# Kernel tuning notes

Measured on AMD Instinct MI355X. Metric: run time of the kernel, lower is better.

## Reference

```python
import jax, jax.numpy as jnp
import numpy as np

IN_F, HID, OUT_F = 171, 1024, 171

def _cond_lst(condition_num, groundtruth_num, seq_len):
    num_cycles = seq_len // (condition_num + groundtruth_num) + 1
    lst = np.zeros((num_cycles, condition_num + groundtruth_num), dtype=np.float32)
    lst[:, :groundtruth_num] = 1.0
    return lst.reshape(-1)[:seq_len]

def setup_inputs() -> dict:
    key = jax.random.key(0)
    ks = jax.random.split(key, 16)
    s = 0.02
    inp = {
        'real_seq': jax.random.normal(ks[0], (128, 128, IN_F), jnp.float32),
        'W_ih1': jax.random.normal(ks[1], (4 * HID, IN_F), jnp.float32) * s,
        'W_hh1': jax.random.normal(ks[2], (4 * HID, HID), jnp.float32) * s,
        'b_ih1': jnp.zeros((4 * HID,), jnp.float32),
        'b_hh1': jnp.zeros((4 * HID,), jnp.float32),
        'W_ih2': jax.random.normal(ks[3], (4 * HID, HID), jnp.float32) * s,
        'W_hh2': jax.random.normal(ks[4], (4 * HID, HID), jnp.float32) * s,
        'b_ih2': jnp.zeros((4 * HID,), jnp.float32),
        'b_hh2': jnp.zeros((4 * HID,), jnp.float32),
        'W_ih3': jax.random.normal(ks[5], (4 * HID, HID), jnp.float32) * s,
        'W_hh3': jax.random.normal(ks[6], (4 * HID, HID), jnp.float32) * s,
        'b_ih3': jnp.zeros((4 * HID,), jnp.float32),
        'b_hh3': jnp.zeros((4 * HID,), jnp.float32),
        'W_dec': jax.random.normal(ks[7], (OUT_F, HID), jnp.float32) * s,
        'b_dec': jnp.zeros((OUT_F,), jnp.float32),
        'condition_num': 5,
        'groundtruth_num': 5,
    }
    return inp

def _lstm_cell(x, h, c, Wih, Whh, bih, bhh):
    # PyTorch LSTMCell: gates ordered i, f, g, o
    g = x @ Wih.T + bih + h @ Whh.T + bhh
    i, f, gg, o = jnp.split(g, 4, axis=-1)
    c2 = jax.nn.sigmoid(f) * c + jax.nn.sigmoid(i) * jnp.tanh(gg)
    h2 = jax.nn.sigmoid(o) * jnp.tanh(c2)
    return h2, c2

def reference(real_seq, W_ih1, W_hh1, b_ih1, b_hh1, W_ih2, W_hh2, b_ih2, b_hh2,
              W_ih3, W_hh3, b_ih3, b_hh3, W_dec, b_dec, condition_num, groundtruth_num):
    B, T, _ = real_seq.shape
    cond = jnp.asarray(_cond_lst(condition_num, groundtruth_num, T))  # [T], 1=use ground truth
    z = jnp.zeros((B, HID), jnp.float32)
    carry0 = (z, z, z, z, z, z, jnp.zeros((B, OUT_F), jnp.float32))
    xs = (jnp.swapaxes(real_seq, 0, 1), cond)  # time-major

    def step(carry, x):
        h0, h1, h2, c0, c1, c2, out_frame = carry
        frame, c_flag = x
        in_frame = jnp.where(c_flag > 0.5, frame, out_frame)
        h0, c0 = _lstm_cell(in_frame, h0, c0, W_ih1, W_hh1, b_ih1, b_hh1)
        h1, c1 = _lstm_cell(h0, h1, c1, W_ih2, W_hh2, b_ih2, b_hh2)
        h2, c2 = _lstm_cell(h1, h2, c2, W_ih3, W_hh3, b_ih3, b_hh3)
        out_frame = h2 @ W_dec.T + b_dec
        return (h0, h1, h2, c0, c1, c2, out_frame), out_frame

    _, out_seq = jax.lax.scan(step, carry0, xs)  # [T, B, OUT_F]
    return jnp.swapaxes(out_seq, 0, 1)  # [B, T, OUT_F]
```

## Files before the change

### kernel.cpp

```cpp
#include <hip/hip_runtime.h>

#define TT 128
#define INF 171

typedef _Float16 half8 __attribute__((ext_vector_type(8)));
typedef float floatx4 __attribute__((ext_vector_type(4)));
typedef unsigned short u16;

#define XBSZ 163840
#define HSZ  131072

#define WAITV(n) asm volatile("s_waitcnt vmcnt(" #n ")" ::: "memory")
#define SCHEDB() __builtin_amdgcn_sched_barrier(0)

__device__ __forceinline__ u16 f2h(float f){
  _Float16 h = (_Float16)f;
  return __builtin_bit_cast(u16, h);
}
__device__ __forceinline__ float sigm(float x){ return 1.f/(1.f+__expf(-x)); }
__device__ __forceinline__ float tanh_(float x){ return 1.f - 2.f/(__expf(2.f*x)+1.f); }

__device__ __forceinline__ void scat_coh(u16* buf, int nch, int b, int k, u16 v){
  u16* p = buf + (size_t)((((b>>4)*nch + (k>>5))*4 + ((k>>3)&3))*16 + (b&15))*8 + (k&7);
  unsigned int vv = v;
  asm volatile("global_store_short %0, %1, off sc0 sc1" :: "v"(p), "v"(vv) : "memory");
}
__device__ __forceinline__ void ld16_coh(half8& d, const u16* p){
  asm volatile("global_load_dwordx4 %0, %1, off sc0 sc1" : "=&v"(d) : "v"(p) : "memory");
}

template<int NB>
__device__ __forceinline__ void issue_pair(const u16* s0, const u16* s1,
    half8* v, int tid, int beat0){
  #pragma unroll
  for (int i=0;i<NB;i++) ld16_coh(v[i],    s0 + (size_t)(beat0+i)*4096 + (size_t)tid*8);
  #pragma unroll
  for (int i=0;i<NB;i++) ld16_coh(v[NB+i], s1 + (size_t)(beat0+i)*4096 + (size_t)tid*8);
}

__global__ __launch_bounds__(256) void prep_w1f(const float* __restrict__ Wih1,
    const float* __restrict__ Whh1, u16* __restrict__ Wf){
  int u = blockIdx.x*256 + threadIdx.x;
  int tile = u / 2560;
  int r = u - tile*2560;
  int kc = r >> 6, l = r & 63;
  int row = (tile>>6)*1024 + (tile&63)*16 + (l&15);
  int k0 = kc*32 + ((l>>4)<<3);
  half8 hv;
  #pragma unroll
  for (int e=0;e<8;e++){
    int k = k0+e;
    float w = 0.f;
    if (k < 171)       w = Wih1[(size_t)row*171 + k];
    else if (k < 1195) w = Whh1[(size_t)row*1024 + (k-171)];
    hv[e] = (_Float16)w;
  }
  *(half8*)&Wf[(size_t)(tile*40 + kc)*512 + (size_t)l*8] = hv;
}

__global__ __launch_bounds__(256) void prep_w23f(const float* __restrict__ Wih2,
    const float* __restrict__ Whh2, const float* __restrict__ Wih3,
    const float* __restrict__ Whh3, u16* __restrict__ W2f, u16* __restrict__ W3f){
  int u = blockIdx.x*256 + threadIdx.x;
  int tile = u >> 12;
  int r = u & 4095;
  int kc = r >> 6, l = r & 63;
  int row = (tile>>6)*1024 + (tile&63)*16 + (l&15);
  int k0 = kc*32 + ((l>>4)<<3);
  half8 h2, h3;
  #pragma unroll
  for (int e=0;e<8;e++){
    int k = k0+e;
    size_t si = (size_t)row*1024 + (k & 1023);
    h2[e] = (_Float16)((k < 1024) ? Wih2[si] : Whh2[si]);
    h3[e] = (_Float16)((k < 1024) ? Wih3[si] : Whh3[si]);
  }
  size_t base = (size_t)(tile*64 + kc)*512 + (size_t)l*8;
  *(half8*)&W2f[base] = h2;
  *(half8*)&W3f[base] = h3;
}

__global__ __launch_bounds__(256) void prep_wdecf(const float* __restrict__ Wdec,
    u16* __restrict__ Wdf){
  int u = blockIdx.x*256 + threadIdx.x;
  int tile = u / 2048;
  int r = u & 2047;
  int kc = r >> 6, l = r & 63;
  int row = tile*16 + (l&15);
  int k0 = kc*32 + ((l>>4)<<3);
  half8 hv;
  #pragma unroll
  for (int e=0;e<8;e++){
    int k = k0+e;
    hv[e] = (_Float16)((row < 171) ? Wdec[(size_t)row*1024 + k] : 0.f);
  }
  *(half8*)&Wdf[(size_t)(tile*32 + kc)*512 + (size_t)l*8] = hv;
}

__global__ __launch_bounds__(256) void prep_misc(
    const float* __restrict__ rseq, const int* __restrict__ gnp,
    const float* __restrict__ bih1, const float* __restrict__ bhh1,
    const float* __restrict__ bih2, const float* __restrict__ bhh2,
    const float* __restrict__ bih3, const float* __restrict__ bhh3,
    const float* __restrict__ bdec,
    u16* __restrict__ Xb1f, u16* __restrict__ Hf, float* __restrict__ cbuf,
    float* __restrict__ b1, float* __restrict__ b2, float* __restrict__ b3,
    float* __restrict__ bd, int* __restrict__ bar)
{
  size_t idx = (size_t)blockIdx.x*256 + threadIdx.x;
  if (idx < 327680){
    int q = (int)(idx / 163840);
    int rem = (int)(idx % 163840);
    int btile = rem / 20480;
    int r2 = rem % 20480;
    int kc = r2 >> 9, r3 = r2 & 511;
    int l = r3 >> 3, e = r3 & 7;
    int b = btile*16 + (l&15);
    int k = kc*32 + ((l>>4)<<3) + e;
    float v = 0.f;
    if (q==0 && k < 171 && *gnp > 0) v = rseq[(size_t)b*TT*INF + k];
    Xb1f[idx] = f2h(v);
    return;
  }
  idx -= 327680;
  if (idx < 786432){ Hf[idx] = 0; return; }
  idx -= 786432;
  if (idx < 393216){ cbuf[idx] = 0.f; return; }
  idx -= 393216;
  if (idx < 12288){
    int which = (int)(idx >> 12), j = (int)(idx & 4095);
    float v = (which==0)? (bih1[j]+bhh1[j]) : (which==1)? (bih2[j]+bhh2[j]) : (bih3[j]+bhh3[j]);
    ((which==0)?b1:(which==1)?b2:b3)[j] = v;
    return;
  }
  idx -= 12288;
  if (idx < 176){ bd[idx] = (idx < 171) ? bdec[idx] : 0.f; return; }
  idx -= 176;
  if (idx < 512) bar[idx] = 0;
}

__device__ __forceinline__ void gridbar(int* __restrict__ bar, int cls, int hv,
                                        int bc, int* s_dead){
  __syncthreads();
  if (threadIdx.x == 0 && !(*s_dead)){
    int* arr = &bar[cls*64 + hv*32];
    int* gen = &bar[256 + cls*32];
    bool released = false;
    int o = __hip_atomic_fetch_add(arr, 1, __ATOMIC_RELAXED, __HIP_MEMORY_SCOPE_AGENT);
    if ((o & 31) == 31){
      int og = __hip_atomic_fetch_add(gen, 1, __ATOMIC_RELAXED, __HIP_MEMORY_SCOPE_AGENT);
      released = (og & 1) == 1;
    }
    if (!released){
      long long t0 = clock64();
      while (__hip_atomic_load(gen, __ATOMIC_RELAXED, __HIP_MEMORY_SCOPE_AGENT) < 2*(bc+1)){
        __builtin_amdgcn_s_sleep(2);
        if (clock64() - t0 > 30000000LL){ *s_dead = 1; break; }
      }
    }
  }
  __syncthreads();
}

template<int KHALF, int GS, bool NT>
__device__ __forceinline__ void gemm_stream(const u16* __restrict__ wp,
    const u16* __restrict__ x0, const u16* __restrict__ x1,
    floatx4& a0, floatx4& a1)
{
  constexpr int NG = KHALF/GS;
  half8 W[2][GS];
  #pragma unroll
  for (int i=0;i<GS;i++)
    W[0][i] = NT ? __builtin_nontemporal_load((const half8*)(wp + (size_t)i*512))
                 : *(const half8*)(wp + (size_t)i*512);
  #pragma unroll
  for (int g8=0; g8<NG; g8++){
    const int cur = g8 & 1, nxt = cur ^ 1;
    if (g8+1 < NG){
      const size_t off = (size_t)(g8+1)*GS*512;
      #pragma unroll
      for (int i=0;i<GS;i++)
        W[nxt][i] = NT ? __builtin_nontemporal_load((const half8*)(wp + off + (size_t)i*512))
                       : *(const half8*)(wp + off + (size_t)i*512);
    }
    #pragma unroll
    for (int i=0;i<GS;i++){
      half8 xv0 = *(const half8*)(x0 + (size_t)(g8*GS+i)*512);
      half8 xv1 = *(const half8*)(x1 + (size_t)(g8*GS+i)*512);
      a0 = __builtin_amdgcn_mfma_f32_16x16x32_f16(W[cur][i], xv0, a0, 0,0,0);
      a1 = __builtin_amdgcn_mfma_f32_16x16x32_f16(W[cur][i], xv1, a1, 0,0,0);
    }
  }
}

__global__ void __launch_bounds__(512,2) acro_persist(
    const u16* __restrict__ W1f, const u16* __restrict__ W2f,
    const u16* __restrict__ W3f, const u16* __restrict__ Wdf,
    u16* __restrict__ Xb1f, u16* __restrict__ Hf,
    const float* __restrict__ b1, const float* __restrict__ b2,
    const float* __restrict__ b3, const float* __restrict__ bd,
    const float* __restrict__ rseq, float* __restrict__ out,
    const int* __restrict__ cnp, const int* __restrict__ gnp, int* __restrict__ bar)
{
  __shared__ u16 XL[65536];
  __shared__ float gb[8][16][33];
  __shared__ int s_dead;
  const int bId = (int)blockIdx.x;
  const int js = (bId & 7)*8 + ((bId >> 5) & 7);
  const int nq = (bId >> 3) & 3;
  const int bh = (bId >> 5) & 1;
  const int tid = (int)threadIdx.x;
  const int w = tid >> 6, l = tid & 63;
  const int g = w >> 1, hf = w & 1;
  const int l15 = l & 15, lq = l >> 4;
  const int uu = tid >> 5, bq = tid & 31;
  const int jj = js*16 + uu, bgg = nq*32 + bq;
  if (tid == 0) s_dead = 0;
  const int gnv = *gnp;
  int P = *cnp + gnv; if (P < 1) P = 1;
  int bc = 0;

  u16* H0[2] = { Hf,          Hf + HSZ   };
  u16* H1[2] = { Hf + 2*HSZ,  Hf + 3*HSZ };
  u16* H2[2] = { Hf + 4*HSZ,  Hf + 5*HSZ };

  float bs1[4], bs2[4], bs3[4];
  #pragma unroll
  for (int q=0;q<4;q++){
    bs1[q] = b1[q*1024 + jj];
    bs2[q] = b2[q*1024 + jj];
    bs3[q] = b3[q*1024 + jj];
  }
  const bool dec_act = (js < 11);
  const int oo = js*16 + uu;
  const float bdr = dec_act ? bd[oo] : 0.f;
  float c0r = 0.f, c1r = 0.f, c2r = 0.f;

  half8 pf1[8], pf2[8], pf3[8];
  issue_pair<4>(Xb1f + (size_t)(nq*2  )*20480,
                Xb1f + (size_t)(nq*2+1)*20480, pf1, tid, 1);

  __syncthreads();
  for (int t=0; t<TT; t++){
    const int pr = t & 1, nx = pr ^ 1;

    {
      const u16* xb = Xb1f + (size_t)pr*XBSZ;
      half8 fr0, fr1;
      ld16_coh(fr0, xb + (size_t)(nq*2  )*20480 + (size_t)tid*8);
      ld16_coh(fr1, xb + (size_t)(nq*2+1)*20480 + (size_t)tid*8);
      WAITV(0);
      SCHEDB();
      *(half8*)&XL[(size_t)tid*8] = fr0;
      *(half8*)&XL[(size_t)5*4096 + (size_t)tid*8] = fr1;
      #pragma unroll
      for (int i=0;i<4;i++){
        *(half8*)&XL[(size_t)(1+i)*4096 + (size_t)tid*8] = pf1[i];
        *(half8*)&XL[(size_t)(6+i)*4096 + (size_t)tid*8] = pf1[4+i];
      }
      __syncthreads();
      const u16* wp = W1f + ((size_t)(g*64 + js)*40 + (size_t)hf*20)*512 + (size_t)(l<<3);
      const u16* x0 = XL + (size_t)hf*10240 + (size_t)(l<<3);
      const u16* x1 = x0 + 20480;
      floatx4 a0{}, a1{};
      gemm_stream<20,4,false>(wp, x0, x1, a0, a1);
      #pragma unroll
      for (int r=0;r<4;r++){
        gb[w][lq*4+r][l15]      = a0[r];
        gb[w][lq*4+r][16 + l15] = a1[r];
      }
      __syncthreads();
      {
        float gi = gb[0][uu][bq] + gb[1][uu][bq] + bs1[0];
        float gf = gb[2][uu][bq] + gb[3][uu][bq] + bs1[1];
        float gg = gb[4][uu][bq] + gb[5][uu][bq] + bs1[2];
        float go = gb[6][uu][bq] + gb[7][uu][bq] + bs1[3];
        float c = sigm(gf)*c0r + sigm(gi)*tanh_(gg);
        c0r = c;
        u16 hb = f2h(sigm(go)*tanh_(c));
        scat_coh(H0[pr], 32, bgg, jj, hb);
        scat_coh(Xb1f + (size_t)nx*XBSZ, 40, bgg, 171 + jj, hb);
      }
      issue_pair<4>(H1[nx] + (size_t)(nq*2  )*16384,
                    H1[nx] + (size_t)(nq*2+1)*16384, pf2, tid, 0);
    }
    WAITV(8);
    gridbar(bar, nq, bh, bc, &s_dead); bc++;

    {
      half8 fr[8];
      issue_pair<4>(H0[pr] + (size_t)(nq*2  )*16384,
                    H0[pr] + (size_t)(nq*2+1)*16384, fr, tid, 0);
      WAITV(0);
      SCHEDB();
      #pragma unroll
      for (int i=0;i<8;i++) *(half8*)&XL[(size_t)i*4096 + (size_t)tid*8] = fr[i];
      #pragma unroll
      for (int i=0;i<8;i++) *(half8*)&XL[32768 + (size_t)i*4096 + (size_t)tid*8] = pf2[i];
      __syncthreads();
      const u16* wp = W2f + ((size_t)(g*64 + js)*64 + (size_t)hf*32)*512 + (size_t)(l<<3);
      const u16* x0 = XL + (size_t)hf*32768 + (size_t)(l<<3);
      const u16* x1 = x0 + 16384;
      floatx4 a0{}, a1{};
      gemm_stream<32,8,false>(wp, x0, x1, a0, a1);
      #pragma unroll
      for (int r=0;r<4;r++){
        gb[w][lq*4+r][l15]      = a0[r];
        gb[w][lq*4+r][16 + l15] = a1[r];
      }
      __syncthreads();
      {
        float gi = gb[0][uu][bq] + gb[1][uu][bq] + bs2[0];
        float gf = gb[2][uu][bq] + gb[3][uu][bq] + bs2[1];
        float gg = gb[4][uu][bq] + gb[5][uu][bq] + bs2[2];
        float go = gb[6][uu][bq] + gb[7][uu][bq] + bs2[3];
        float c = sigm(gf)*c1r + sigm(gi)*tanh_(gg);
        c1r = c;
        u16 hb = f2h(sigm(go)*tanh_(c));
        scat_coh(H1[pr], 32, bgg, jj, hb);
      }
      issue_pair<4>(H2[nx] + (size_t)(nq*2  )*16384,
                    H2[nx] + (size_t)(nq*2+1)*16384, pf3, tid, 0);
    }
    WAITV(8);
    gridbar(bar, nq, bh, bc, &s_dead); bc++;

    {
      half8 fr[8];
      issue_pair<4>(H1[pr] + (size_t)(nq*2  )*16384,
                    H1[pr] + (size_t)(nq*2+1)*16384, fr, tid, 0);
      WAITV(0);
      SCHEDB();
      #pragma unroll
      for (int i=0;i<8;i++) *(half8*)&XL[(size_t)i*4096 + (size_t)tid*8] = fr[i];
      #pragma unroll
      for (int i=0;i<8;i++) *(half8*)&XL[32768 + (size_t)i*4096 + (size_t)tid*8] = pf3[i];
      __syncthreads();
      const u16* wp = W3f + ((size_t)(g*64 + js)*64 + (size_t)hf*32)*512 + (size_t)(l<<3);
      const u16* x0 = XL + (size_t)hf*32768 + (size_t)(l<<3);
      const u16* x1 = x0 + 16384;
      floatx4 a0{}, a1{};
      gemm_stream<32,8,true>(wp, x0, x1, a0, a1);
      #pragma unroll
      for (int r=0;r<4;r++){
        gb[w][lq*4+r][l15]      = a0[r];
        gb[w][lq*4+r][16 + l15] = a1[r];
      }
      __syncthreads();
      {
        float gi = gb[0][uu][bq] + gb[1][uu][bq] + bs3[0];
        float gf = gb[2][uu][bq] + gb[3][uu][bq] + bs3[1];
        float gg = gb[4][uu][bq] + gb[5][uu][bq] + bs3[2];
        float go = gb[6][uu][bq] + gb[7][uu][bq] + bs3[3];
        float c = sigm(gf)*c2r + sigm(gi)*tanh_(gg);
        c2r = c;
        u16 hb = f2h(sigm(go)*tanh_(c));
        scat_coh(H2[pr], 32, bgg, jj, hb);
      }
    }
    WAITV(0);
    gridbar(bar, nq, bh, bc, &s_dead); bc++;

    if (dec_act){
      half8 fd[8];
      issue_pair<4>(H2[pr] + (size_t)(nq*2  )*16384,
                    H2[pr] + (size_t)(nq*2+1)*16384, fd, tid, 0);
      WAITV(0);
      SCHEDB();
      #pragma unroll
      for (int i=0;i<8;i++) *(half8*)&XL[(size_t)i*4096 + (size_t)tid*8] = fd[i];
      __syncthreads();
      const u16* wp = Wdf + (size_t)(js*32 + w*4)*512 + (size_t)(l<<3);
      const u16* x0 = XL + (size_t)(w*4)*512 + (size_t)(l<<3);
      const u16* x1 = x0 + 16384;
      floatx4 d0{}, d1{};
      #pragma unroll
      for (int i=0;i<4;i++){
        half8 wv  = *(const half8*)(wp + (size_t)i*512);
        half8 a0v = *(const half8*)(x0 + (size_t)i*512);
        half8 a1v = *(const half8*)(x1 + (size_t)i*512);
        d0 = __builtin_amdgcn_mfma_f32_16x16x32_f16(wv, a0v, d0, 0,0,0);
        d1 = __builtin_amdgcn_mfma_f32_16x16x32_f16(wv, a1v, d1, 0,0,0);
      }
      #pragma unroll
      for (int r=0;r<4;r++){
        gb[w][lq*4+r][l15]      = d0[r];
        gb[w][lq*4+r][16 + l15] = d1[r];
      }
      __syncthreads();
      const int nf = (((t+1) % P) < gnv) ? 1 : 0;
      if (oo < 171){
        float v = bdr;
        #pragma unroll
        for (int i=0;i<8;i++) v += gb[i][uu][bq];
        out[((size_t)bgg*TT + t)*INF + oo] = v;
        if (t+1 < TT){
          float src = nf ? rseq[((size_t)bgg*TT + (t+1))*INF + oo] : v;
          scat_coh(Xb1f + (size_t)nx*XBSZ, 40, bgg, oo, f2h(src));
        }
      }
    }
    if (t+1 < TT){
      const u16* xbn = Xb1f + (size_t)nx*XBSZ;
      issue_pair<4>(xbn + (size_t)(nq*2  )*20480,
                    xbn + (size_t)(nq*2+1)*20480, pf1, tid, 1);
      WAITV(8);
    } else {
      WAITV(0);
    }
    gridbar(bar, nq, bh, bc, &s_dead); bc++;
  }
}

extern "C" void kernel_launch(void* const* d_in, const int* in_sizes, int n_in,
                              void* d_out, int out_size, void* d_ws, size_t ws_size,
                              hipStream_t stream)
{
  const float* rseq = (const float*)d_in[0];
  const float* Wih1 = (const float*)d_in[1];
  const float* Whh1 = (const float*)d_in[2];
  const float* bih1 = (const float*)d_in[3];
  const float* bhh1 = (const float*)d_in[4];
  const float* Wih2 = (const float*)d_in[5];
  const float* Whh2 = (const float*)d_in[6];
  const float* bih2 = (const float*)d_in[7];
  const float* bhh2 = (const float*)d_in[8];
  const float* Wih3 = (const float*)d_in[9];
  const float* Whh3 = (const float*)d_in[10];
  const float* bih3 = (const float*)d_in[11];
  const float* bhh3 = (const float*)d_in[12];
  const float* Wdec = (const float*)d_in[13];
  const float* bdec = (const float*)d_in[14];
  const int* cn = (const int*)d_in[15];
  const int* gn = (const int*)d_in[16];
  float* out = (float*)d_out;

  char* p = (char*)d_ws;
  auto take = [&](size_t n){ void* r = (void*)p; p += (n + 255) & ~(size_t)255; return r; };
  u16* W1f  = (u16*)take(5242880UL*2);
  u16* W2f  = (u16*)take(8388608UL*2);
  u16* W3f  = (u16*)take(8388608UL*2);
  u16* Wdf  = (u16*)take(180224UL*2);
  u16* Xb1f = (u16*)take(327680UL*2);
  u16* Hf   = (u16*)take(786432UL*2);
  float* cbuf = (float*)take(393216UL*4);
  float* b1 = (float*)take(4096*4);
  float* b2 = (float*)take(4096*4);
  float* b3 = (float*)take(4096*4);
  float* bd = (float*)take(176*4);
  int* bar  = (int*)take(512*4);
  if ((size_t)(p - (char*)d_ws) > ws_size) return;

  prep_w1f  <<<2560,256,0,stream>>>(Wih1, Whh1, W1f);
  prep_w23f <<<4096,256,0,stream>>>(Wih2, Whh2, Wih3, Whh3, W2f, W3f);
  prep_wdecf<<<88,  256,0,stream>>>(Wdec, Wdf);
  prep_misc <<<5939,256,0,stream>>>(rseq, gn, bih1,bhh1,bih2,bhh2,bih3,bhh3,bdec,
                                    Xb1f, Hf, cbuf, b1,b2,b3,bd, bar);

  acro_persist<<<256,512,0,stream>>>(W1f, W2f, W3f, Wdf, Xb1f, Hf,
                                     b1, b2, b3, bd, rseq, out, cn, gn, bar);
}
```

Baseline: 4.867 ms.

## Split persistent LSTM grid into 512 blocks each owning 16 batch rows

```diff
diff --git a/kernel.cpp b/kernel.cpp
--- a/kernel.cpp
+++ b/kernel.cpp
@@ -10,7 +10,7 @@
 #define XBSZ 163840
 #define HSZ  131072
 
-#define WAITV(n) asm volatile("s_waitcnt vmcnt(" #n ")" ::: "memory")
+#define WAITV0() asm volatile("s_waitcnt vmcnt(0)" ::: "memory")
 #define SCHEDB() __builtin_amdgcn_sched_barrier(0)
 
 __device__ __forceinline__ u16 f2h(float f){
@@ -27,15 +27,6 @@
 }
 __device__ __forceinline__ void ld16_coh(half8& d, const u16* p){
   asm volatile("global_load_dwordx4 %0, %1, off sc0 sc1" : "=&v"(d) : "v"(p) : "memory");
-}
-
-template<int NB>
-__device__ __forceinline__ void issue_pair(const u16* s0, const u16* s1,
-    half8* v, int tid, int beat0){
-  #pragma unroll
-  for (int i=0;i<NB;i++) ld16_coh(v[i],    s0 + (size_t)(beat0+i)*4096 + (size_t)tid*8);
-  #pragma unroll
-  for (int i=0;i<NB;i++) ld16_coh(v[NB+i], s1 + (size_t)(beat0+i)*4096 + (size_t)tid*8);
 }
 
 __global__ __launch_bounds__(256) void prep_w1f(const float* __restrict__ Wih1,
@@ -136,15 +127,15 @@
   idx -= 12288;
   if (idx < 176){ bd[idx] = (idx < 171) ? bdec[idx] : 0.f; return; }
   idx -= 176;
-  if (idx < 512) bar[idx] = 0;
+  if (idx < 1024) bar[idx] = 0;
 }
 
 __device__ __forceinline__ void gridbar(int* __restrict__ bar, int cls, int hv,
                                         int bc, int* s_dead){
   __syncthreads();
   if (threadIdx.x == 0 && !(*s_dead)){
-    int* arr = &bar[cls*64 + hv*32];
-    int* gen = &bar[256 + cls*32];
+    int* arr = &bar[(cls*2 + hv)*32];
+    int* gen = &bar[512 + cls*32];
     bool released = false;
     int o = __hip_atomic_fetch_add(arr, 1, __ATOMIC_RELAXED, __HIP_MEMORY_SCOPE_AGENT);
     if ((o & 31) == 31){
@@ -162,17 +153,39 @@
   __syncthreads();
 }
 
-template<int KHALF, int GS, bool NT>
-__device__ __forceinline__ void gemm_stream(const u16* __restrict__ wp,
-    const u16* __restrict__ x0, const u16* __restrict__ x1,
-    floatx4& a0, floatx4& a1)
+template<int NB>
+__device__ __forceinline__ void stage_n(const u16* s0, u16* XL, int tid, int lb0){
+  half8 v[NB];
+  #pragma unroll
+  for (int i=0;i<NB;i++) ld16_coh(v[i], s0 + (size_t)i*4096 + (size_t)tid*8);
+  WAITV0();
+  SCHEDB();
+  #pragma unroll
+  for (int i=0;i<NB;i++) *(half8*)&XL[(size_t)(lb0+i)*4096 + (size_t)tid*8] = v[i];
+}
+__device__ __forceinline__ void stage_44(const u16* sf, const u16* ss,
+                                         u16* XL, int tid){
+  half8 v[8];
+  #pragma unroll
+  for (int i=0;i<4;i++) ld16_coh(v[i],   sf + (size_t)i*4096 + (size_t)tid*8);
+  #pragma unroll
+  for (int i=0;i<4;i++) ld16_coh(v[4+i], ss + (size_t)i*4096 + (size_t)tid*8);
+  WAITV0();
+  SCHEDB();
+  #pragma unroll
+  for (int i=0;i<8;i++) *(half8*)&XL[(size_t)i*4096 + (size_t)tid*8] = v[i];
+}
+
+template<int KHALF>
+__device__ __forceinline__ void gemm1(const u16* __restrict__ wp,
+    const u16* __restrict__ x0, floatx4& a0)
 {
+  constexpr int GS = 4;
   constexpr int NG = KHALF/GS;
   half8 W[2][GS];
   #pragma unroll
   for (int i=0;i<GS;i++)
-    W[0][i] = NT ? __builtin_nontemporal_load((const half8*)(wp + (size_t)i*512))
-                 : *(const half8*)(wp + (size_t)i*512);
+    W[0][i] = *(const half8*)(wp + (size_t)i*512);
   #pragma unroll
   for (int g8=0; g8<NG; g8++){
     const int cur = g8 & 1, nxt = cur ^ 1;
@@ -180,20 +193,17 @@
       const size_t off = (size_t)(g8+1)*GS*512;
       #pragma unroll
       for (int i=0;i<GS;i++)
-        W[nxt][i] = NT ? __builtin_nontemporal_load((const half8*)(wp + off + (size_t)i*512))
-                       : *(const half8*)(wp + off + (size_t)i*512);
+        W[nxt][i] = *(const half8*)(wp + off + (size_t)i*512);
     }
     #pragma unroll
     for (int i=0;i<GS;i++){
       half8 xv0 = *(const half8*)(x0 + (size_t)(g8*GS+i)*512);
-      half8 xv1 = *(const half8*)(x1 + (size_t)(g8*GS+i)*512);
       a0 = __builtin_amdgcn_mfma_f32_16x16x32_f16(W[cur][i], xv0, a0, 0,0,0);
-      a1 = __builtin_amdgcn_mfma_f32_16x16x32_f16(W[cur][i], xv1, a1, 0,0,0);
-    }
-  }
-}
-
-__global__ void __launch_bounds__(512,2) acro_persist(
+    }
+  }
+}
+
+__global__ void __launch_bounds__(512,4) acro_persist(
     const u16* __restrict__ W1f, const u16* __restrict__ W2f,
     const u16* __restrict__ W3f, const u16* __restrict__ Wdf,
     u16* __restrict__ Xb1f, u16* __restrict__ Hf,
@@ -202,19 +212,23 @@
     const float* __restrict__ rseq, float* __restrict__ out,
     const int* __restrict__ cnp, const int* __restrict__ gnp, int* __restrict__ bar)
 {
-  __shared__ u16 XL[65536];
-  __shared__ float gb[8][16][33];
+  __shared__ u16 XL[32768];
+  __shared__ float gb[8][16][17];
   __shared__ int s_dead;
   const int bId = (int)blockIdx.x;
-  const int js = (bId & 7)*8 + ((bId >> 5) & 7);
-  const int nq = (bId >> 3) & 3;
-  const int bh = (bId >> 5) & 1;
+  const int lo = bId & 255;
+  const int js = (lo & 7)*8 + ((lo >> 5) & 7);
+  const int q2 = (lo >> 3) & 3;
+  const int half = bId >> 8;
+  const int ct = q2*2 + half;
+  const int hv = (lo >> 5) & 1;
   const int tid = (int)threadIdx.x;
   const int w = tid >> 6, l = tid & 63;
   const int g = w >> 1, hf = w & 1;
   const int l15 = l & 15, lq = l >> 4;
-  const int uu = tid >> 5, bq = tid & 31;
-  const int jj = js*16 + uu, bgg = nq*32 + bq;
+  const int uu = (tid >> 4) & 15, bq = tid & 15;
+  const bool ep = (tid < 256);
+  const int jj = js*16 + uu, bgg = ct*16 + bq;
   if (tid == 0) s_dead = 0;
   const int gnv = *gnp;
   int P = *cnp + gnv; if (P < 1) P = 1;
@@ -232,45 +246,32 @@
     bs3[q] = b3[q*1024 + jj];
   }
   const bool dec_act = (js < 11);
-  const int oo = js*16 + uu;
+  const int oo = jj;
   const float bdr = dec_act ? bd[oo] : 0.f;
   float c0r = 0.f, c1r = 0.f, c2r = 0.f;
 
-  half8 pf1[8], pf2[8], pf3[8];
-  issue_pair<4>(Xb1f + (size_t)(nq*2  )*20480,
-                Xb1f + (size_t)(nq*2+1)*20480, pf1, tid, 1);
+  const size_t xoff = (size_t)ct*20480;
+  const size_t hoff = (size_t)ct*16384;
+
+  const u16* wp1 = W1f + ((size_t)(g*64 + js)*40 + (size_t)hf*20)*512 + (size_t)(l<<3);
+  const u16* wp2 = W2f + ((size_t)(g*64 + js)*64 + (size_t)hf*32)*512 + (size_t)(l<<3);
+  const u16* wp3 = W3f + ((size_t)(g*64 + js)*64 + (size_t)hf*32)*512 + (size_t)(l<<3);
+  const u16* wpd = Wdf + (size_t)(js*32 + w*4)*512 + (size_t)(l<<3);
 
   __syncthreads();
   for (int t=0; t<TT; t++){
     const int pr = t & 1, nx = pr ^ 1;
 
     {
-      const u16* xb = Xb1f + (size_t)pr*XBSZ;
-      half8 fr0, fr1;
-      ld16_coh(fr0, xb + (size_t)(nq*2  )*20480 + (size_t)tid*8);
-      ld16_coh(fr1, xb + (size_t)(nq*2+1)*20480 + (size_t)tid*8);
-      WAITV(0);
-      SCHEDB();
-      *(half8*)&XL[(size_t)tid*8] = fr0;
-      *(half8*)&XL[(size_t)5*4096 + (size_t)tid*8] = fr1;
-      #pragma unroll
-      for (int i=0;i<4;i++){
-        *(half8*)&XL[(size_t)(1+i)*4096 + (size_t)tid*8] = pf1[i];
-        *(half8*)&XL[(size_t)(6+i)*4096 + (size_t)tid*8] = pf1[4+i];
-      }
-      __syncthreads();
-      const u16* wp = W1f + ((size_t)(g*64 + js)*40 + (size_t)hf*20)*512 + (size_t)(l<<3);
+      stage_n<5>(Xb1f + (size_t)pr*XBSZ + xoff, XL, tid, 0);
+      __syncthreads();
       const u16* x0 = XL + (size_t)hf*10240 + (size_t)(l<<3);
-      const u16* x1 = x0 + 20480;
-      floatx4 a0{}, a1{};
-      gemm_stream<20,4,false>(wp, x0, x1, a0, a1);
-      #pragma unroll
-      for (int r=0;r<4;r++){
-        gb[w][lq*4+r][l15]      = a0[r];
-        gb[w][lq*4+r][16 + l15] = a1[r];
-      }
-      __syncthreads();
-      {
+      floatx4 a0{};
+      gemm1<20>(wp1, x0, a0);
+      #pragma unroll
+      for (int r=0;r<4;r++) gb[w][lq*4+r][l15] = a0[r];
+      __syncthreads();
+      if (ep){
         float gi = gb[0][uu][bq] + gb[1][uu][bq] + bs1[0];
         float gf = gb[2][uu][bq] + gb[3][uu][bq] + bs1[1];
         float gg = gb[4][uu][bq] + gb[5][uu][bq] + bs1[2];
@@ -281,35 +282,20 @@
         scat_coh(H0[pr], 32, bgg, jj, hb);
         scat_coh(Xb1f + (size_t)nx*XBSZ, 40, bgg, 171 + jj, hb);
       }
-      issue_pair<4>(H1[nx] + (size_t)(nq*2  )*16384,
-                    H1[nx] + (size_t)(nq*2+1)*16384, pf2, tid, 0);
-    }
-    WAITV(8);
-    gridbar(bar, nq, bh, bc, &s_dead); bc++;
+    }
+    WAITV0();
+    gridbar(bar, ct, hv, bc, &s_dead); bc++;
 
     {
-      half8 fr[8];
-      issue_pair<4>(H0[pr] + (size_t)(nq*2  )*16384,
-                    H0[pr] + (size_t)(nq*2+1)*16384, fr, tid, 0);
-      WAITV(0);
-      SCHEDB();
-      #pragma unroll
-      for (int i=0;i<8;i++) *(half8*)&XL[(size_t)i*4096 + (size_t)tid*8] = fr[i];
-      #pragma unroll
-      for (int i=0;i<8;i++) *(half8*)&XL[32768 + (size_t)i*4096 + (size_t)tid*8] = pf2[i];
-      __syncthreads();
-      const u16* wp = W2f + ((size_t)(g*64 + js)*64 + (size_t)hf*32)*512 + (size_t)(l<<3);
-      const u16* x0 = XL + (size_t)hf*32768 + (size_t)(l<<3);
-      const u16* x1 = x0 + 16384;
-      floatx4 a0{}, a1{};
-      gemm_stream<32,8,false>(wp, x0, x1, a0, a1);
-      #pragma unroll
-      for (int r=0;r<4;r++){
-        gb[w][lq*4+r][l15]      = a0[r];
-        gb[w][lq*4+r][16 + l15] = a1[r];
-      }
-      __syncthreads();
-      {
+      stage_44(H0[pr] + hoff, H1[nx] + hoff, XL, tid);
+      __syncthreads();
+      const u16* x0 = XL + (size_t)hf*16384 + (size_t)(l<<3);
+      floatx4 a0{};
+      gemm1<32>(wp2, x0, a0);
+      #pragma unroll
+      for (int r=0;r<4;r++) gb[w][lq*4+r][l15] = a0[r];
+      __syncthreads();
+      if (ep){
         float gi = gb[0][uu][bq] + gb[1][uu][bq] + bs2[0];
         float gf = gb[2][uu][bq] + gb[3][uu][bq] + bs2[1];
         float gg = gb[4][uu][bq] + gb[5][uu][bq] + bs2[2];
@@ -319,35 +305,20 @@
         u16 hb = f2h(sigm(go)*tanh_(c));
         scat_coh(H1[pr], 32, bgg, jj, hb);
       }
-      issue_pair<4>(H2[nx] + (size_t)(nq*2  )*16384,
-                    H2[nx] + (size_t)(nq*2+1)*16384, pf3, tid, 0);
-    }
-    WAITV(8);
-    gridbar(bar, nq, bh, bc, &s_dead); bc++;
+    }
+    WAITV0();
+    gridbar(bar, ct, hv, bc, &s_dead); bc++;
 
     {
-      half8 fr[8];
-      issue_pair<4>(H1[pr] + (size_t)(nq*2  )*16384,
-                    H1[pr] + (size_t)(nq*2+1)*16384, fr, tid, 0);
-      WAITV(0);
-      SCHEDB();
-      #pragma unroll
-      for (int i=0;i<8;i++) *(half8*)&XL[(size_t)i*4096 + (size_t)tid*8] = fr[i];
-      #pragma unroll
-      for (int i=0;i<8;i++) *(half8*)&XL[32768 + (size_t)i*4096 + (size_t)tid*8] = pf3[i];
-      __syncthreads();
-      const u16* wp = W3f + ((size_t)(g*64 + js)*64 + (size_t)hf*32)*512 + (size_t)(l<<3);
-      const u16* x0 = XL + (size_t)hf*32768 + (size_t)(l<<3);
-      const u16* x1 = x0 + 16384;
-      floatx4 a0{}, a1{};
-      gemm_stream<32,8,true>(wp, x0, x1, a0, a1);
-      #pragma unroll
-      for (int r=0;r<4;r++){
-        gb[w][lq*4+r][l15]      = a0[r];
-        gb[w][lq*4+r][16 + l15] = a1[r];
-      }
-      __syncthreads();
-      {
+      stage_44(H1[pr] + hoff, H2[nx] + hoff, XL, tid);
+      __syncthreads();
+      const u16* x0 = XL + (size_t)hf*16384 + (size_t)(l<<3);
+      floatx4 a0{};
+      gemm1<32>(wp3, x0, a0);
+      #pragma unroll
+      for (int r=0;r<4;r++) gb[w][lq*4+r][l15] = a0[r];
+      __syncthreads();
+      if (ep){
         float gi = gb[0][uu][bq] + gb[1][uu][bq] + bs3[0];
         float gf = gb[2][uu][bq] + gb[3][uu][bq] + bs3[1];
         float gg = gb[4][uu][bq] + gb[5][uu][bq] + bs3[2];
@@ -358,38 +329,25 @@
         scat_coh(H2[pr], 32, bgg, jj, hb);
       }
     }
-    WAITV(0);
-    gridbar(bar, nq, bh, bc, &s_dead); bc++;
+    WAITV0();
+    gridbar(bar, ct, hv, bc, &s_dead); bc++;
 
     if (dec_act){
-      half8 fd[8];
-      issue_pair<4>(H2[pr] + (size_t)(nq*2  )*16384,
-                    H2[pr] + (size_t)(nq*2+1)*16384, fd, tid, 0);
-      WAITV(0);
-      SCHEDB();
-      #pragma unroll
-      for (int i=0;i<8;i++) *(half8*)&XL[(size_t)i*4096 + (size_t)tid*8] = fd[i];
-      __syncthreads();
-      const u16* wp = Wdf + (size_t)(js*32 + w*4)*512 + (size_t)(l<<3);
+      stage_n<4>(H2[pr] + hoff, XL, tid, 0);
+      __syncthreads();
       const u16* x0 = XL + (size_t)(w*4)*512 + (size_t)(l<<3);
-      const u16* x1 = x0 + 16384;
-      floatx4 d0{}, d1{};
+      floatx4 d0{};
       #pragma unroll
       for (int i=0;i<4;i++){
-        half8 wv  = *(const half8*)(wp + (size_t)i*512);
+        half8 wv  = *(const half8*)(wpd + (size_t)i*512);
         half8 a0v = *(const half8*)(x0 + (size_t)i*512);
-        half8 a1v = *(const half8*)(x1 + (size_t)i*512);
         d0 = __builtin_amdgcn_mfma_f32_16x16x32_f16(wv, a0v, d0, 0,0,0);
-        d1 = __builtin_amdgcn_mfma_f32_16x16x32_f16(wv, a1v, d1, 0,0,0);
-      }
-      #pragma unroll
-      for (int r=0;r<4;r++){
-        gb[w][lq*4+r][l15]      = d0[r];
-        gb[w][lq*4+r][16 + l15] = d1[r];
-      }
+      }
+      #pragma unroll
+      for (int r=0;r<4;r++) gb[w][lq*4+r][l15] = d0[r];
       __syncthreads();
       const int nf = (((t+1) % P) < gnv) ? 1 : 0;
-      if (oo < 171){
+      if (ep && oo < 171){
         float v = bdr;
         #pragma unroll
         for (int i=0;i<8;i++) v += gb[i][uu][bq];
@@ -400,15 +358,8 @@
         }
       }
     }
-    if (t+1 < TT){
-      const u16* xbn = Xb1f + (size_t)nx*XBSZ;
-      issue_pair<4>(xbn + (size_t)(nq*2  )*20480,
-                    xbn + (size_t)(nq*2+1)*20480, pf1, tid, 1);
-      WAITV(8);
-    } else {
-      WAITV(0);
-    }
-    gridbar(bar, nq, bh, bc, &s_dead); bc++;
+    WAITV0();
+    gridbar(bar, ct, hv, bc, &s_dead); bc++;
   }
 }
 
@@ -448,15 +399,15 @@
   float* b2 = (float*)take(4096*4);
   float* b3 = (float*)take(4096*4);
   float* bd = (float*)take(176*4);
-  int* bar  = (int*)take(512*4);
+  int* bar  = (int*)take(1024*4);
   if ((size_t)(p - (char*)d_ws) > ws_size) return;
 
   prep_w1f  <<<2560,256,0,stream>>>(Wih1, Whh1, W1f);
   prep_w23f <<<4096,256,0,stream>>>(Wih2, Whh2, Wih3, Whh3, W2f, W3f);
   prep_wdecf<<<88,  256,0,stream>>>(Wdec, Wdf);
-  prep_misc <<<5939,256,0,stream>>>(rseq, gn, bih1,bhh1,bih2,bhh2,bih3,bhh3,bdec,
+  prep_misc <<<5941,256,0,stream>>>(rseq, gn, bih1,bhh1,bih2,bhh2,bih3,bhh3,bdec,
                                     Xb1f, Hf, cbuf, b1,b2,b3,bd, bar);
 
-  acro_persist<<<256,512,0,stream>>>(W1f, W2f, W3f, Wdf, Xb1f, Hf,
+  acro_persist<<<512,512,0,stream>>>(W1f, W2f, W3f, Wdf, Xb1f, Hf,
                                      b1, b2, b3, bd, rseq, out, cn, gn, bar);
 }
```

Result: slower. 6.210 ms (+27.6%).

## Prefetch next layer's weights across grid barriers using a 4-deep register ring

Applied to the files above, without the earlier changes.

```diff
diff --git a/kernel.cpp b/kernel.cpp
--- a/kernel.cpp
+++ b/kernel.cpp
@@ -28,6 +28,9 @@
 __device__ __forceinline__ void ld16_coh(half8& d, const u16* p){
   asm volatile("global_load_dwordx4 %0, %1, off sc0 sc1" : "=&v"(d) : "v"(p) : "memory");
 }
+__device__ __forceinline__ void ld16_c(half8& d, const u16* p){
+  asm volatile("global_load_dwordx4 %0, %1, off" : "=&v"(d) : "v"(p) : "memory");
+}
 
 template<int NB>
 __device__ __forceinline__ void issue_pair(const u16* s0, const u16* s1,
@@ -36,6 +39,15 @@
   for (int i=0;i<NB;i++) ld16_coh(v[i],    s0 + (size_t)(beat0+i)*4096 + (size_t)tid*8);
   #pragma unroll
   for (int i=0;i<NB;i++) ld16_coh(v[NB+i], s1 + (size_t)(beat0+i)*4096 + (size_t)tid*8);
+}
+
+template<bool COH>
+__device__ __forceinline__ void wgrp(half8* Ws, const u16* wp, int grp){
+  #pragma unroll
+  for (int i=0;i<4;i++){
+    const u16* p = wp + (size_t)grp*2048 + (size_t)i*512;
+    if (COH) ld16_coh(Ws[i], p); else ld16_c(Ws[i], p);
+  }
 }
 
 __global__ __launch_bounds__(256) void prep_w1f(const float* __restrict__ Wih1,
@@ -162,34 +174,29 @@
   __syncthreads();
 }
 
-template<int KHALF, int GS, bool NT>
-__device__ __forceinline__ void gemm_stream(const u16* __restrict__ wp,
+template<int NG, bool COH>
+__device__ __forceinline__ void gemm_ring(const u16* __restrict__ wp,
     const u16* __restrict__ x0, const u16* __restrict__ x1,
-    floatx4& a0, floatx4& a1)
+    floatx4& a0, floatx4& a1, half8 (&W)[4][4])
 {
-  constexpr int NG = KHALF/GS;
-  half8 W[2][GS];
-  #pragma unroll
-  for (int i=0;i<GS;i++)
-    W[0][i] = NT ? __builtin_nontemporal_load((const half8*)(wp + (size_t)i*512))
-                 : *(const half8*)(wp + (size_t)i*512);
-  #pragma unroll
-  for (int g8=0; g8<NG; g8++){
-    const int cur = g8 & 1, nxt = cur ^ 1;
-    if (g8+1 < NG){
-      const size_t off = (size_t)(g8+1)*GS*512;
-      #pragma unroll
-      for (int i=0;i<GS;i++)
-        W[nxt][i] = NT ? __builtin_nontemporal_load((const half8*)(wp + off + (size_t)i*512))
-                       : *(const half8*)(wp + off + (size_t)i*512);
+  #pragma unroll
+  for (int g=0; g<NG; g++){
+    if (g >= 2){
+      const int rem = (g+4 <= NG-1) ? 3 : (NG-1-g);
+      if (rem >= 3)      { WAITV(12); }
+      else if (rem == 2) { WAITV(8); }
+      else if (rem == 1) { WAITV(4); }
+      else               { WAITV(0); }
+      SCHEDB();
     }
     #pragma unroll
-    for (int i=0;i<GS;i++){
-      half8 xv0 = *(const half8*)(x0 + (size_t)(g8*GS+i)*512);
-      half8 xv1 = *(const half8*)(x1 + (size_t)(g8*GS+i)*512);
-      a0 = __builtin_amdgcn_mfma_f32_16x16x32_f16(W[cur][i], xv0, a0, 0,0,0);
-      a1 = __builtin_amdgcn_mfma_f32_16x16x32_f16(W[cur][i], xv1, a1, 0,0,0);
-    }
+    for (int i=0;i<4;i++){
+      half8 xv0 = *(const half8*)(x0 + (size_t)(g*4+i)*512);
+      half8 xv1 = *(const half8*)(x1 + (size_t)(g*4+i)*512);
+      a0 = __builtin_amdgcn_mfma_f32_16x16x32_f16(W[g&3][i], xv0, a0, 0,0,0);
+      a1 = __builtin_amdgcn_mfma_f32_16x16x32_f16(W[g&3][i], xv1, a1, 0,0,0);
+    }
+    if (g+4 < NG) wgrp<COH>(W[g&3], wp, g+4);
   }
 }
 
@@ -224,6 +231,11 @@
   u16* H1[2] = { Hf + 2*HSZ,  Hf + 3*HSZ };
   u16* H2[2] = { Hf + 4*HSZ,  Hf + 5*HSZ };
 
+  const u16* wp1 = W1f + ((size_t)(g*64 + js)*40 + (size_t)hf*20)*512 + (size_t)(l<<3);
+  const u16* wp2 = W2f + ((size_t)(g*64 + js)*64 + (size_t)hf*32)*512 + (size_t)(l<<3);
+  const u16* wp3 = W3f + ((size_t)(g*64 + js)*64 + (size_t)hf*32)*512 + (size_t)(l<<3);
+  const u16* wpd = Wdf + (size_t)(js*32 + w*4)*512 + (size_t)(l<<3);
+
   float bs1[4], bs2[4], bs3[4];
   #pragma unroll
   for (int q=0;q<4;q++){
@@ -237,8 +249,11 @@
   float c0r = 0.f, c1r = 0.f, c2r = 0.f;
 
   half8 pf1[8], pf2[8], pf3[8];
+  half8 Wr[4][4];
   issue_pair<4>(Xb1f + (size_t)(nq*2  )*20480,
                 Xb1f + (size_t)(nq*2+1)*20480, pf1, tid, 1);
+  wgrp<false>(Wr[0], wp1, 0);
+  wgrp<false>(Wr[1], wp1, 1);
 
   __syncthreads();
   for (int t=0; t<TT; t++){
@@ -249,7 +264,9 @@
       half8 fr0, fr1;
       ld16_coh(fr0, xb + (size_t)(nq*2  )*20480 + (size_t)tid*8);
       ld16_coh(fr1, xb + (size_t)(nq*2+1)*20480 + (size_t)tid*8);
-      WAITV(0);
+      wgrp<false>(Wr[2], wp1, 2);
+      wgrp<false>(Wr[3], wp1, 3);
+      WAITV(8);
       SCHEDB();
       *(half8*)&XL[(size_t)tid*8] = fr0;
       *(half8*)&XL[(size_t)5*4096 + (size_t)tid*8] = fr1;
@@ -259,11 +276,10 @@
         *(half8*)&XL[(size_t)(6+i)*4096 + (size_t)tid*8] = pf1[4+i];
       }
       __syncthreads();
-      const u16* wp = W1f + ((size_t)(g*64 + js)*40 + (size_t)hf*20)*512 + (size_t)(l<<3);
       const u16* x0 = XL + (size_t)hf*10240 + (size_t)(l<<3);
       const u16* x1 = x0 + 20480;
       floatx4 a0{}, a1{};
-      gemm_stream<20,4,false>(wp, x0, x1, a0, a1);
+      gemm_ring<5,false>(wp1, x0, x1, a0, a1, Wr);
       #pragma unroll
       for (int r=0;r<4;r++){
         gb[w][lq*4+r][l15]      = a0[r];
@@ -283,26 +299,29 @@
       }
       issue_pair<4>(H1[nx] + (size_t)(nq*2  )*16384,
                     H1[nx] + (size_t)(nq*2+1)*16384, pf2, tid, 0);
-    }
-    WAITV(8);
+      wgrp<false>(Wr[0], wp2, 0);
+      wgrp<false>(Wr[1], wp2, 1);
+    }
+    WAITV(16);
     gridbar(bar, nq, bh, bc, &s_dead); bc++;
 
     {
       half8 fr[8];
       issue_pair<4>(H0[pr] + (size_t)(nq*2  )*16384,
                     H0[pr] + (size_t)(nq*2+1)*16384, fr, tid, 0);
-      WAITV(0);
+      wgrp<false>(Wr[2], wp2, 2);
+      wgrp<false>(Wr[3], wp2, 3);
+      WAITV(8);
       SCHEDB();
       #pragma unroll
       for (int i=0;i<8;i++) *(half8*)&XL[(size_t)i*4096 + (size_t)tid*8] = fr[i];
       #pragma unroll
       for (int i=0;i<8;i++) *(half8*)&XL[32768 + (size_t)i*4096 + (size_t)tid*8] = pf2[i];
       __syncthreads();
-      const u16* wp = W2f + ((size_t)(g*64 + js)*64 + (size_t)hf*32)*512 + (size_t)(l<<3);
       const u16* x0 = XL + (size_t)hf*32768 + (size_t)(l<<3);
       const u16* x1 = x0 + 16384;
       floatx4 a0{}, a1{};
-      gemm_stream<32,8,false>(wp, x0, x1, a0, a1);
+      gemm_ring<8,false>(wp2, x0, x1, a0, a1, Wr);
       #pragma unroll
       for (int r=0;r<4;r++){
         gb[w][lq*4+r][l15]      = a0[r];
@@ -321,26 +340,29 @@
       }
       issue_pair<4>(H2[nx] + (size_t)(nq*2  )*16384,
                     H2[nx] + (size_t)(nq*2+1)*16384, pf3, tid, 0);
-    }
-    WAITV(8);
+      wgrp<true>(Wr[0], wp3, 0);
+      wgrp<true>(Wr[1], wp3, 1);
+    }
+    WAITV(16);
     gridbar(bar, nq, bh, bc, &s_dead); bc++;
 
     {
       half8 fr[8];
       issue_pair<4>(H1[pr] + (size_t)(nq*2  )*16384,
                     H1[pr] + (size_t)(nq*2+1)*16384, fr, tid, 0);
-      WAITV(0);
+      wgrp<true>(Wr[2], wp3, 2);
+      wgrp<true>(Wr[3], wp3, 3);
+      WAITV(8);
       SCHEDB();
       #pragma unroll
       for (int i=0;i<8;i++) *(half8*)&XL[(size_t)i*4096 + (size_t)tid*8] = fr[i];
       #pragma unroll
       for (int i=0;i<8;i++) *(half8*)&XL[32768 + (size_t)i*4096 + (size_t)tid*8] = pf3[i];
       __syncthreads();
-      const u16* wp = W3f + ((size_t)(g*64 + js)*64 + (size_t)hf*32)*512 + (size_t)(l<<3);
       const u16* x0 = XL + (size_t)hf*32768 + (size_t)(l<<3);
       const u16* x1 = x0 + 16384;
       floatx4 a0{}, a1{};
-      gemm_stream<32,8,true>(wp, x0, x1, a0, a1);
+      gemm_ring<8,true>(wp3, x0, x1, a0, a1, Wr);
       #pragma unroll
       for (int r=0;r<4;r++){
         gb[w][lq*4+r][l15]      = a0[r];
@@ -370,13 +392,12 @@
       #pragma unroll
       for (int i=0;i<8;i++) *(half8*)&XL[(size_t)i*4096 + (size_t)tid*8] = fd[i];
       __syncthreads();
-      const u16* wp = Wdf + (size_t)(js*32 + w*4)*512 + (size_t)(l<<3);
       const u16* x0 = XL + (size_t)(w*4)*512 + (size_t)(l<<3);
       const u16* x1 = x0 + 16384;
       floatx4 d0{}, d1{};
       #pragma unroll
       for (int i=0;i<4;i++){
-        half8 wv  = *(const half8*)(wp + (size_t)i*512);
+        half8 wv  = *(const half8*)(wpd + (size_t)i*512);
         half8 a0v = *(const half8*)(x0 + (size_t)i*512);
         half8 a1v = *(const half8*)(x1 + (size_t)i*512);
         d0 = __builtin_amdgcn_mfma_f32_16x16x32_f16(wv, a0v, d0, 0,0,0);
@@ -404,7 +425,9 @@
       const u16* xbn = Xb1f + (size_t)nx*XBSZ;
       issue_pair<4>(xbn + (size_t)(nq*2  )*20480,
                     xbn + (size_t)(nq*2+1)*20480, pf1, tid, 1);
-      WAITV(8);
+      wgrp<false>(Wr[0], wp1, 0);
+      wgrp<false>(Wr[1], wp1, 1);
+      WAITV(16);
     } else {
       WAITV(0);
     }
```

Result: slower. 5.732 ms (+17.8%).
